# Kernel optimization log

Measured on AMD Instinct MI355X. Metric: run time of the kernel, lower is better.

Reference implementation:

```python
import jax, jax.numpy as jnp
import numpy as np

NEG_SLOPE = 0.2


def setup_inputs() -> dict:
    key = jax.random.key(0)
    k1, k2, k3, k4, k5 = jax.random.split(key, 5)
    N, F_in, F_out, H, D = 4096, 256, 256, 4, 64
    x = jax.random.normal(k1, (N, F_in), dtype=jnp.float32)
    adj = jax.random.normal(k2, (N, N), dtype=jnp.float32)  # ~half entries > 0 -> edges
    W = jax.random.normal(k3, (F_out, F_in), dtype=jnp.float32) * (1.0 / np.sqrt(F_in))
    a_src = jax.random.normal(k4, (H, D), dtype=jnp.float32) * 0.1
    a_dst = jax.random.normal(k5, (H, D), dtype=jnp.float32) * 0.1
    return {"x": x, "adj": adj, "W": W, "a_src": a_src, "a_dst": a_dst}


def reference(x, adj, W, a_src, a_dst):
    N = x.shape[0]
    H, D = a_src.shape
    # linear projection (torch Linear: x @ W.T), reshape to heads
    h = (x @ W.T).reshape(N, H, D)                      # [N, H, D]
    attn_src = jnp.einsum('nhd,hd->nh', h, a_src)       # [N, H]
    attn_dst = jnp.einsum('nhd,hd->nh', h, a_dst)       # [N, H]
    scores = attn_src[:, None, :] + attn_dst[None, :, :]  # [N, N, H]
    scores = jnp.where(scores >= 0, scores, NEG_SLOPE * scores)  # leaky_relu(0.2)
    mask = (adj > 0)[:, :, None]                        # [N, N, 1]
    scores = jnp.where(mask, scores, -jnp.inf)
    attn = jax.nn.softmax(scores, axis=1)               # softmax over neighbors j
    attn = jnp.nan_to_num(attn, nan=0.0)                # fully-masked rows -> 0
    weighted = attn * adj[:, :, None]                   # weight by adjacency values
    out = jnp.einsum('ijh,jhd->ihd', weighted, h)       # [N, H, D]
    return out.reshape(N, H * D)
```

## Files before the change

### kernel.cpp

```cpp
#include <hip/hip_runtime.h>
#include <stdint.h>

#define NN 4096
#define FF 256
#define HH 4
#define DD 64
#define NEG 0.2f
#define LOG2E 1.4426950408889634f

#define ITILE 32
#define NS 8
#define JR (NN / NS)
#define CJ 128
#define NCH (JR / CJ)
#define NB (NN / 8)

typedef __attribute__((ext_vector_type(8))) short short8;
typedef __attribute__((ext_vector_type(4))) float f32x4;
typedef __attribute__((ext_vector_type(16))) float f32x16;

__device__ __forceinline__ uint16_t bf16_rh(float f) {
    uint32_t u = __float_as_uint(f);
    return (uint16_t)((u + 0x8000u) >> 16);
}
__device__ __forceinline__ uint32_t cvtpk(float lo, float hi) {
    uint32_t r;
    asm("v_cvt_pk_bf16_f32 %0, %1, %2" : "=v"(r) : "v"(lo), "v"(hi));
    return r;
}

__global__ __launch_bounds__(256) void gemm_h(const float* __restrict__ x,
                                              const float* __restrict__ W,
                                              const float* __restrict__ a_src,
                                              const float* __restrict__ a_dst,
                                              float* __restrict__ s,
                                              float* __restrict__ T_T,
                                              uint16_t* __restrict__ Bf,
                                              float* __restrict__ pden) {
    __shared__ uint16_t xs[64][264];
    __shared__ uint16_t wsl[64][264];
    const int tid = threadIdx.x;
    if (blockIdx.y == 0) pden[blockIdx.x * 256 + tid] = 0.f;
    const int i0g = blockIdx.x * 64;
    const int f0 = blockIdx.y * 64;
    const int hh = blockIdx.y;
    const float* xsrc = x + (size_t)i0g * FF;
    const float* wsrc = W + (size_t)f0 * FF;
    {
        const int rw = tid >> 6, c4 = (tid & 63) * 4;
#pragma unroll
        for (int p = 0; p < 16; p++) {
            float4 vx = ((const float4*)xsrc)[p * 256 + tid];
            float4 vw = ((const float4*)wsrc)[p * 256 + tid];
            *(uint2*)&xs[p * 4 + rw][c4] =
                make_uint2(cvtpk(vx.x, vx.y), cvtpk(vx.z, vx.w));
            *(uint2*)&wsl[p * 4 + rw][c4] =
                make_uint2(cvtpk(vw.x, vw.y), cvtpk(vw.z, vw.w));
        }
    }
    __syncthreads();
    const int w = tid >> 6, l = tid & 63;
    const int m = l & 15, q = l >> 4;
    const int i0 = i0g + w * 16;
    f32x4 acc[4];
#pragma unroll
    for (int n = 0; n < 4; n++)
#pragma unroll
        for (int r = 0; r < 4; r++) acc[n][r] = 0.f;
    const uint16_t* ax = &xs[w * 16 + m][q * 8];
#pragma unroll
    for (int k0 = 0; k0 < 8; k0++) {
        short8 af = *(const short8*)(ax + k0 * 32);
#pragma unroll
        for (int n = 0; n < 4; n++) {
            short8 bf = *(const short8*)&wsl[n * 16 + m][k0 * 32 + q * 8];
            acc[n] = __builtin_amdgcn_mfma_f32_16x16x32_bf16(af, bf, acc[n], 0, 0, 0);
        }
    }
    const float* as = a_src + hh * DD;
    const float* ad = a_dst + hh * DD;
    float av[4], dv[4];
#pragma unroll
    for (int n = 0; n < 4; n++) { av[n] = as[n * 16 + m]; dv[n] = ad[n * 16 + m]; }
#pragma unroll
    for (int r = 0; r < 4; r++) {
        float vs = 0.f, vd = 0.f;
#pragma unroll
        for (int n = 0; n < 4; n++) {
            vs = fmaf(acc[n][r], av[n], vs);
            vd = fmaf(acc[n][r], dv[n], vd);
        }
#pragma unroll
        for (int off = 1; off < 16; off <<= 1) {
            vs += __shfl_xor(vs, off, 64);
            vd += __shfl_xor(vd, off, 64);
        }
        if (m == 0) {
            const int i = i0 + q * 4 + r;
            s[(size_t)i * HH + hh] = vs * LOG2E;
            T_T[(size_t)hh * NN + i] = vd * LOG2E;
        }
    }
    const int iblk = blockIdx.x * 8 + w * 2 + (q >> 1);
    const int jjo  = (q & 1) * 4;
#pragma unroll
    for (int n = 0; n < 4; n++) {
        *(uint2*)(Bf + (((size_t)hh * NB + iblk) * 64 + n * 16 + m) * 8 + jjo) =
            make_uint2(cvtpk(acc[n][0], acc[n][1]), cvtpk(acc[n][2], acc[n][3]));
    }
}

__global__ __launch_bounds__(256, 4) void gat_main(
    const float* __restrict__ adj, const uint16_t* __restrict__ Bf,
    const float* __restrict__ s, const float* __restrict__ T_T,
    float* __restrict__ pden, uint16_t* __restrict__ part) {
    __shared__ float adj_s[2][CJ][32];
    const int tid = threadIdx.x;
    const int w = tid >> 6, l = tid & 63;
    const int m = l & 31, q = l >> 5;
    constexpr int NWG = (NN / ITILE) * NS;
    const int orig = blockIdx.y * (NN / ITILE) + blockIdx.x;
    const int swz = (orig & 7) * (NWG / 8) + (orig >> 3);
    const int i0 = (swz & (NN / ITILE - 1)) * ITILE;
    const int sl = swz / (NN / ITILE);
    const int jb = sl * JR;

    const float sS = s[(size_t)(i0 + m) * HH + w];
    const float sB = NEG * sS;
    float den = 0.f;
    f32x16 acc0, acc1;
#pragma unroll
    for (int r = 0; r < 16; r++) { acc0[r] = 0.f; acc1[r] = 0.f; }
    const float* trow = T_T + (size_t)w * NN;
    const uint16_t* bbase = Bf + (size_t)w * NB * 512;

    const int is = tid >> 3, r7 = tid & 7, j16 = r7 * 16;
    const int colw = is ^ (r7 << 2);
    const float* arow = adj + (size_t)(i0 + is) * NN + j16;

    float4 pre[4];
#pragma unroll
    for (int c4 = 0; c4 < 4; c4++) pre[c4] = *(const float4*)(arow + jb + c4 * 4);
#pragma unroll
    for (int c4 = 0; c4 < 4; c4++) {
        adj_s[0][j16 + c4 * 4 + 0][colw] = pre[c4].x;
        adj_s[0][j16 + c4 * 4 + 1][colw] = pre[c4].y;
        adj_s[0][j16 + c4 * 4 + 2][colw] = pre[c4].z;
        adj_s[0][j16 + c4 * 4 + 3][colw] = pre[c4].w;
    }
#pragma unroll
    for (int c4 = 0; c4 < 4; c4++) pre[c4] = *(const float4*)(arow + jb + CJ + c4 * 4);
    __syncthreads();

    for (int c = 0; c < NCH; ++c) {
        const int jc = jb + c * CJ;
        const int cur = c & 1;
        if (c + 1 < NCH) {
            const int nb = cur ^ 1;
#pragma unroll
            for (int c4 = 0; c4 < 4; c4++) {
                adj_s[nb][j16 + c4 * 4 + 0][colw] = pre[c4].x;
                adj_s[nb][j16 + c4 * 4 + 1][colw] = pre[c4].y;
                adj_s[nb][j16 + c4 * 4 + 2][colw] = pre[c4].z;
                adj_s[nb][j16 + c4 * 4 + 3][colw] = pre[c4].w;
            }
            if (c + 2 < NCH) {
#pragma unroll
                for (int c4 = 0; c4 < 4; c4++)
                    pre[c4] = *(const float4*)(arow + jc + 2 * CJ + c4 * 4);
            }
        }
#pragma unroll
        for (int kk = 0; kk < CJ; kk += 16) {
            const int jg = jc + kk + q * 8;
            const int jblk = ((jc + kk) >> 3) + q;
            const int cmv = m ^ (((kk >> 4) & 7) << 2);
            float4 t0 = *(const float4*)(trow + jg);
            float4 t1 = *(const float4*)(trow + jg + 4);
            short8 bf0 = *(const short8*)(bbase + (size_t)jblk * 512 + m * 8);
            short8 bf1 = *(const short8*)(bbase + (size_t)jblk * 512 + (32 + m) * 8);
            float tt[8] = {t0.x, t0.y, t0.z, t0.w, t1.x, t1.y, t1.z, t1.w};
            union { uint32_t u[4]; short8 v; } afu;
#pragma unroll
            for (int jj = 0; jj < 8; jj += 2) {
                const int rr = kk + q * 8 + jj;
                float a0 = adj_s[cur][rr][cmv], a1 = adj_s[cur][rr + 1][cmv];
                float tv0 = tt[jj], tv1 = tt[jj + 1];
                float x0 = sS + tv0,           x1 = sS + tv1;
                float z0 = fmaf(NEG, tv0, sB), z1 = fmaf(NEG, tv1, sB);
                float lr0 = fmaxf(x0, z0), lr1 = fmaxf(x1, z1);
                float e0, e1;
                asm("v_exp_f32 %0, %1" : "=v"(e0) : "v"(lr0));
                asm("v_exp_f32 %0, %1" : "=v"(e1) : "v"(lr1));
                e0 = (a0 > 0.f) ? e0 : 0.f;
                e1 = (a1 > 0.f) ? e1 : 0.f;
                den += e0 + e1;
                afu.u[jj >> 1] = cvtpk(e0 * a0, e1 * a1);
            }
            acc0 = __builtin_amdgcn_mfma_f32_32x32x16_bf16(afu.v, bf0, acc0, 0, 0, 0);
            acc1 = __builtin_amdgcn_mfma_f32_32x32x16_bf16(afu.v, bf1, acc1, 0, 0, 0);
        }
        __syncthreads();
    }
    den += __shfl_down(den, 32, 64);
    if (l < 32) atomicAdd(&pden[(size_t)(i0 + m) * HH + w], den);
    uint16_t* pbase = part + (size_t)sl * NN * FF;
#pragma unroll
    for (int reg = 0; reg < 16; reg++) {
        int row = (reg & 3) + 8 * (reg >> 2) + 4 * q;
        pbase[(size_t)(i0 + row) * FF + w * DD + m]      = bf16_rh(acc0[reg]);
        pbase[(size_t)(i0 + row) * FF + w * DD + 32 + m] = bf16_rh(acc1[reg]);
    }
}

__global__ __launch_bounds__(256) void finalize(const uint16_t* __restrict__ part,
                                                const float* __restrict__ pden,
                                                float* __restrict__ out) {
    const int i = blockIdx.x * 8 + (threadIdx.x >> 5);
    const int f8 = (threadIdx.x & 31) * 8;
    float acc[8];
#pragma unroll
    for (int e = 0; e < 8; e++) acc[e] = 0.f;
#pragma unroll
    for (int sl = 0; sl < NS; sl++) {
        union { short8 v; uint16_t u[8]; } b;
        b.v = *(const short8*)(part + (size_t)sl * NN * FF + (size_t)i * FF + f8);
#pragma unroll
        for (int e = 0; e < 8; e++)
            acc[e] += __uint_as_float(((uint32_t)b.u[e]) << 16);
    }
    float d = pden[(size_t)i * HH + (f8 >> 6)];
    float inv = (d > 0.f) ? 1.f / d : 0.f;
    *(float4*)(out + (size_t)i * FF + f8) =
        make_float4(acc[0] * inv, acc[1] * inv, acc[2] * inv, acc[3] * inv);
    *(float4*)(out + (size_t)i * FF + f8 + 4) =
        make_float4(acc[4] * inv, acc[5] * inv, acc[6] * inv, acc[7] * inv);
}

extern "C" void kernel_launch(void* const* d_in, const int* in_sizes, int n_in,
                              void* d_out, int out_size, void* d_ws, size_t ws_size,
                              hipStream_t stream) {
    const float* x     = (const float*)d_in[0];
    const float* adj   = (const float*)d_in[1];
    const float* W     = (const float*)d_in[2];
    const float* a_src = (const float*)d_in[3];
    const float* a_dst = (const float*)d_in[4];
    float* out = (float*)d_out;

    char* ws = (char*)d_ws;
    uint16_t* Bf   = (uint16_t*)ws;
    float*    s    = (float*)(ws + (2u << 20));
    float*    T_T  = s + (size_t)NN * HH;
    float*    pden = T_T + (size_t)HH * NN;
    uint16_t* part = (uint16_t*)(ws + (3u << 20));

    gemm_h<<<dim3(NN / 64, HH), 256, 0, stream>>>(x, W, a_src, a_dst, s, T_T, Bf, pden);
    gat_main<<<dim3(NN / ITILE, NS), 256, 0, stream>>>(adj, Bf, s, T_T, pden, part);
    finalize<<<NN / 8, 256, 0, stream>>>(part, pden, out);
}
```

Before: 130.4 us.

## Split neighbor range into 16 slices, halve chunk size, stage T_T in shared memory

The main GAT kernel is templated on the number of j-slices and launched with 16 slices when the workspace is large enough, falling back to 8. This doubles the grid to spread the adjacency stream over more workgroups. The chunk size drops from 128 to 64 so each thread prefetches fewer registers. Attention destination terms are now staged through a double-buffered shared array instead of being read from global memory per k-step, and the LDS swizzle index is adjusted to match. The cost is twice as many bf16 partial buffers for finalize to read and sum, plus more atomic adds on the denominators.

After: 133.1 us. +2.1%, slower.

```diff
diff --git a/kernel.cpp b/kernel.cpp
--- a/kernel.cpp
+++ b/kernel.cpp
@@ -9,10 +9,7 @@
 #define LOG2E 1.4426950408889634f
 
 #define ITILE 32
-#define NS 8
-#define JR (NN / NS)
-#define CJ 128
-#define NCH (JR / CJ)
+#define CJ 64
 #define NB (NN / 8)
 
 typedef __attribute__((ext_vector_type(8))) short short8;
@@ -110,20 +107,24 @@
     }
 }
 
+template<int NSt>
 __global__ __launch_bounds__(256, 4) void gat_main(
     const float* __restrict__ adj, const uint16_t* __restrict__ Bf,
     const float* __restrict__ s, const float* __restrict__ T_T,
     float* __restrict__ pden, uint16_t* __restrict__ part) {
+    constexpr int JRt = NN / NSt;
+    constexpr int NCH = JRt / CJ;
     __shared__ float adj_s[2][CJ][32];
+    __shared__ float ts[2][HH][CJ];
     const int tid = threadIdx.x;
     const int w = tid >> 6, l = tid & 63;
     const int m = l & 31, q = l >> 5;
-    constexpr int NWG = (NN / ITILE) * NS;
+    constexpr int NWG = (NN / ITILE) * NSt;
     const int orig = blockIdx.y * (NN / ITILE) + blockIdx.x;
     const int swz = (orig & 7) * (NWG / 8) + (orig >> 3);
     const int i0 = (swz & (NN / ITILE - 1)) * ITILE;
     const int sl = swz / (NN / ITILE);
-    const int jb = sl * JR;
+    const int jb = sl * JRt;
 
     const float sS = s[(size_t)(i0 + m) * HH + w];
     const float sB = NEG * sS;
@@ -131,25 +132,24 @@
     f32x16 acc0, acc1;
 #pragma unroll
     for (int r = 0; r < 16; r++) { acc0[r] = 0.f; acc1[r] = 0.f; }
-    const float* trow = T_T + (size_t)w * NN;
     const uint16_t* bbase = Bf + (size_t)w * NB * 512;
-
-    const int is = tid >> 3, r7 = tid & 7, j16 = r7 * 16;
+    const float* tsrc = T_T + (size_t)w * NN + l;
+
+    const int is = tid >> 3, r7 = tid & 7, j8 = r7 * 8;
     const int colw = is ^ (r7 << 2);
-    const float* arow = adj + (size_t)(i0 + is) * NN + j16;
-
-    float4 pre[4];
-#pragma unroll
-    for (int c4 = 0; c4 < 4; c4++) pre[c4] = *(const float4*)(arow + jb + c4 * 4);
-#pragma unroll
-    for (int c4 = 0; c4 < 4; c4++) {
-        adj_s[0][j16 + c4 * 4 + 0][colw] = pre[c4].x;
-        adj_s[0][j16 + c4 * 4 + 1][colw] = pre[c4].y;
-        adj_s[0][j16 + c4 * 4 + 2][colw] = pre[c4].z;
-        adj_s[0][j16 + c4 * 4 + 3][colw] = pre[c4].w;
-    }
-#pragma unroll
-    for (int c4 = 0; c4 < 4; c4++) pre[c4] = *(const float4*)(arow + jb + CJ + c4 * 4);
+    const float* arow = adj + (size_t)(i0 + is) * NN + j8;
+
+    float4 p0 = *(const float4*)(arow + jb);
+    float4 p1 = *(const float4*)(arow + jb + 4);
+    float tp = tsrc[jb];
+    adj_s[0][j8 + 0][colw] = p0.x; adj_s[0][j8 + 1][colw] = p0.y;
+    adj_s[0][j8 + 2][colw] = p0.z; adj_s[0][j8 + 3][colw] = p0.w;
+    adj_s[0][j8 + 4][colw] = p1.x; adj_s[0][j8 + 5][colw] = p1.y;
+    adj_s[0][j8 + 6][colw] = p1.z; adj_s[0][j8 + 7][colw] = p1.w;
+    ts[0][w][l] = tp;
+    p0 = *(const float4*)(arow + jb + CJ);
+    p1 = *(const float4*)(arow + jb + CJ + 4);
+    tp = tsrc[jb + CJ];
     __syncthreads();
 
     for (int c = 0; c < NCH; ++c) {
@@ -157,26 +157,24 @@
         const int cur = c & 1;
         if (c + 1 < NCH) {
             const int nb = cur ^ 1;
-#pragma unroll
-            for (int c4 = 0; c4 < 4; c4++) {
-                adj_s[nb][j16 + c4 * 4 + 0][colw] = pre[c4].x;
-                adj_s[nb][j16 + c4 * 4 + 1][colw] = pre[c4].y;
-                adj_s[nb][j16 + c4 * 4 + 2][colw] = pre[c4].z;
-                adj_s[nb][j16 + c4 * 4 + 3][colw] = pre[c4].w;
+            adj_s[nb][j8 + 0][colw] = p0.x; adj_s[nb][j8 + 1][colw] = p0.y;
+            adj_s[nb][j8 + 2][colw] = p0.z; adj_s[nb][j8 + 3][colw] = p0.w;
+            adj_s[nb][j8 + 4][colw] = p1.x; adj_s[nb][j8 + 5][colw] = p1.y;
+            adj_s[nb][j8 + 6][colw] = p1.z; adj_s[nb][j8 + 7][colw] = p1.w;
+            ts[nb][w][l] = tp;
+            if (c + 2 < NCH) {
+                p0 = *(const float4*)(arow + jc + 2 * CJ);
+                p1 = *(const float4*)(arow + jc + 2 * CJ + 4);
+                tp = tsrc[jc + 2 * CJ];
             }
-            if (c + 2 < NCH) {
-#pragma unroll
-                for (int c4 = 0; c4 < 4; c4++)
-                    pre[c4] = *(const float4*)(arow + jc + 2 * CJ + c4 * 4);
-            }
         }
 #pragma unroll
         for (int kk = 0; kk < CJ; kk += 16) {
-            const int jg = jc + kk + q * 8;
             const int jblk = ((jc + kk) >> 3) + q;
-            const int cmv = m ^ (((kk >> 4) & 7) << 2);
-            float4 t0 = *(const float4*)(trow + jg);
-            float4 t1 = *(const float4*)(trow + jg + 4);
+            const int cmv = m ^ ((((kk >> 3) + q) & 7) << 2);
+            const float* tptr = &ts[cur][w][kk + q * 8];
+            float4 t0 = *(const float4*)tptr;
+            float4 t1 = *(const float4*)(tptr + 4);
             short8 bf0 = *(const short8*)(bbase + (size_t)jblk * 512 + m * 8);
             short8 bf1 = *(const short8*)(bbase + (size_t)jblk * 512 + (32 + m) * 8);
             float tt[8] = {t0.x, t0.y, t0.z, t0.w, t1.x, t1.y, t1.z, t1.w};
@@ -213,6 +211,7 @@
     }
 }
 
+template<int NSt>
 __global__ __launch_bounds__(256) void finalize(const uint16_t* __restrict__ part,
                                                 const float* __restrict__ pden,
                                                 float* __restrict__ out) {
@@ -222,7 +221,7 @@
 #pragma unroll
     for (int e = 0; e < 8; e++) acc[e] = 0.f;
 #pragma unroll
-    for (int sl = 0; sl < NS; sl++) {
+    for (int sl = 0; sl < NSt; sl++) {
         union { short8 v; uint16_t u[8]; } b;
         b.v = *(const short8*)(part + (size_t)sl * NN * FF + (size_t)i * FF + f8);
 #pragma unroll
@@ -255,6 +254,11 @@
     uint16_t* part = (uint16_t*)(ws + (3u << 20));
 
     gemm_h<<<dim3(NN / 64, HH), 256, 0, stream>>>(x, W, a_src, a_dst, s, T_T, Bf, pden);
-    gat_main<<<dim3(NN / ITILE, NS), 256, 0, stream>>>(adj, Bf, s, T_T, pden, part);
-    finalize<<<NN / 8, 256, 0, stream>>>(part, pden, out);
-}
+    if (ws_size >= (3u << 20) + (size_t)16 * NN * FF * sizeof(uint16_t)) {
+        gat_main<16><<<dim3(NN / ITILE, 16), 256, 0, stream>>>(adj, Bf, s, T_T, pden, part);
+        finalize<16><<<NN / 8, 256, 0, stream>>>(part, pden, out);
+    } else {
+        gat_main<8><<<dim3(NN / ITILE, 8), 256, 0, stream>>>(adj, Bf, s, T_T, pden, part);
+        finalize<8><<<NN / 8, 256, 0, stream>>>(part, pden, out);
+    }
+}
```
